# Kernel tuning notes

Measured on AMD Instinct MI355X. Metric: run time of the kernel, lower is better.

Reference implementation:

```python
import jax, jax.numpy as jnp
import numpy as np


def setup_inputs() -> dict:
    key = jax.random.key(0)
    k1, k2, k3, k4 = jax.random.split(key, 4)
    B, N_LEAVES, D_IN, L, C = 64, 512, 512, 5, 4
    n_nodes = 2 * N_LEAVES - 1  # heap layout: node i has children 2i+1, 2i+2
    h = jax.random.normal(k1, (B, n_nodes, D_IN), dtype=jnp.float32)
    W = jax.random.normal(k2, (D_IN, L * C), dtype=jnp.float32) * (1.0 / np.sqrt(D_IN))
    b = jax.random.normal(k3, (L * C,), dtype=jnp.float32) * 0.02
    trans = jax.random.normal(k4, (L, L, L, C, C, C), dtype=jnp.float32) * 0.1
    return {"h": h, "W": W, "b": b, "trans": trans}


def reference(h, W, b, trans):
    """Batched inside algorithm of BinaryTreeLatentVariable.forward.

    h: [B, n_nodes, D] node hidden states (complete binary tree, heap order).
    Returns root inside score [B, L, C].
    """
    B, n_nodes, _ = h.shape
    L = trans.shape[0]
    C = trans.shape[3]
    n_leaves = (n_nodes + 1) // 2
    depth = int(np.log2(n_leaves))

    # Emission: state_weight_layer applied to every node at once.
    sw = (h @ W + b).reshape(B, n_nodes, L, C)  # [B, N, L, C]

    # Leaves: in_weight = state_weight. Internal slots overwritten bottom-up.
    in_w = sw
    for d in range(depth - 1, -1, -1):  # level-synchronous, bottom-up
        start, end = 2 ** d - 1, 2 ** (d + 1) - 1  # internal nodes of this level
        l = in_w[:, 2 * start + 1:2 * end:2]        # [B, m, L, C] left children
        r = in_w[:, 2 * start + 2:2 * end + 1:2]    # [B, m, L, C] right children
        p = sw[:, start:end]                        # [B, m, L, C] parent emission
        # score[b,m, pL,lL,rL, pc,lc,rc]
        score = (p[:, :, :, None, None, :, None, None]
                 + l[:, :, None, :, None, None, :, None]
                 + r[:, :, None, None, :, None, None, :]
                 + trans)
        new = jax.nn.logsumexp(score, axis=(3, 4, 6, 7))  # marginalize children
        in_w = in_w.at[:, start:end].set(new)
    return in_w[:, 0]  # root inside score [B, L, C]
```

## Files before the change

kernel.cpp:

```cpp
#include <hip/hip_runtime.h>
#include <hip/hip_bf16.h>
#include <math.h>

#define NB      64
#define NNODES  1023
#define LC      20
#define DIN     512
#define NROWS   (NB * NNODES)
#define ET_PAD  404

#define BM      64
#define SCP     21

typedef unsigned short u16;
typedef short bf16x8 __attribute__((ext_vector_type(8)));
typedef float f32x4  __attribute__((ext_vector_type(4)));

__device__ __forceinline__ u16 f2bf(float f) {
    unsigned x = __float_as_uint(f);
    return (u16)((x + 0x7FFFu + ((x >> 16) & 1u)) >> 16);
}

__global__ __launch_bounds__(256) void prep_kernel(
    const float* __restrict__ trans, const float* __restrict__ W,
    float* __restrict__ ET, u16* __restrict__ Bfrag)
{
    int t = blockIdx.x * 256 + threadIdx.x;
    if (t < 8000) {
        int q   = t % 20;
        int rem = t / 20;
        int j   = rem % 20;
        int i   = rem / 20;
        int ll = i >> 2, cl = i & 3;
        int lr = j >> 2, cr = j & 3;
        int lp = q >> 2, cp = q & 3;
        int src = ((((lp * 5 + ll) * 5 + lr) * 4 + cp) * 4 + cl) * 4 + cr;
        ET[q * ET_PAD + i * 20 + j] = expf(trans[src]);
    }
    if (t < 1280) {
        int col, kb;
        if (t < 1024) {
            int lane = t & 63, cg = t >> 6;
            col = lane & 15;
            kb  = cg * 32 + ((lane >> 4) & 3) * 8;
        } else {
            int idx = t - 1024;
            int cg = idx >> 4, g = (idx >> 2) & 3, c = idx & 3;
            col = 16 + c;
            kb  = cg * 32 + g * 8;
        }
        unsigned e[8];
        #pragma unroll
        for (int j = 0; j < 8; ++j)
            e[j] = (unsigned)f2bf(W[(kb + j) * LC + col]);
        uint4 v;
        v.x = e[0] | (e[1] << 16); v.y = e[2] | (e[3] << 16);
        v.z = e[4] | (e[5] << 16); v.w = e[6] | (e[7] << 16);
        ((uint4*)Bfrag)[t] = v;
    }
}

__global__ __launch_bounds__(256, 5) void gemm_kernel(
    const float* __restrict__ h, const u16* __restrict__ Bfrag,
    const float* __restrict__ bias, float* __restrict__ buf)
{
    __shared__ uint4 Bs[1280];
    __shared__ float scT[BM * SCP];
    const int t    = threadIdx.x;
    const int lane = t & 63;
    const int wv   = t >> 6;
    const size_t row0 = (size_t)blockIdx.x * BM;

    Bs[t] = ((const uint4*)Bfrag)[t];
    Bs[t + 256] = ((const uint4*)Bfrag)[t + 256];
    Bs[t + 512] = ((const uint4*)Bfrag)[t + 512];
    Bs[t + 768] = ((const uint4*)Bfrag)[t + 768];
    Bs[t + 1024] = ((const uint4*)Bfrag)[t + 1024];

    const float4* ap4 = (const float4*)
        (h + (row0 + wv * 16 + (lane & 15)) * DIN + ((lane >> 4) << 3));

    f32x4 acc0 = {0.f,0.f,0.f,0.f}, acc1 = {0.f,0.f,0.f,0.f};
    const uint4 z4 = make_uint4(0u, 0u, 0u, 0u);

    float4 pa0 = ap4[0], pb0 = ap4[1];
    float4 pa1 = ap4[8], pb1 = ap4[9];

    asm volatile("s_waitcnt lgkmcnt(0)" ::: "memory");
    __builtin_amdgcn_s_barrier();

    #pragma unroll
    for (int c = 0; c < 16; ++c) {
        float4 x0, x1;
        if (c & 1) { x0 = pa1; x1 = pb1; }
        else       { x0 = pa0; x1 = pb0; }
        if (c + 2 < 16) {
            if (c & 1) { pa1 = ap4[(c + 2) * 8]; pb1 = ap4[(c + 2) * 8 + 1]; }
            else       { pa0 = ap4[(c + 2) * 8]; pb0 = ap4[(c + 2) * 8 + 1]; }
        }
        unsigned e0 = (unsigned)f2bf(x0.x) | ((unsigned)f2bf(x0.y) << 16);
        unsigned e1 = (unsigned)f2bf(x0.z) | ((unsigned)f2bf(x0.w) << 16);
        unsigned e2 = (unsigned)f2bf(x1.x) | ((unsigned)f2bf(x1.y) << 16);
        unsigned e3 = (unsigned)f2bf(x1.z) | ((unsigned)f2bf(x1.w) << 16);
        uint4 au = make_uint4(e0, e1, e2, e3);
        bf16x8 af = __builtin_bit_cast(bf16x8, au);

        uint4 b0 = Bs[c * 64 + lane];
        uint4 b1 = Bs[1024 + c * 16 + ((lane >> 4) << 2) + (lane & 3)];
        if ((lane & 15) >= 4) b1 = z4;

        acc0 = __builtin_amdgcn_mfma_f32_16x16x32_bf16(
            af, __builtin_bit_cast(bf16x8, b0), acc0, 0, 0, 0);
        acc1 = __builtin_amdgcn_mfma_f32_16x16x32_bf16(
            af, __builtin_bit_cast(bf16x8, b1), acc1, 0, 0, 0);
    }

    {
        int col0 = lane & 15;
        int r0   = wv * 16 + ((lane >> 4) << 2);
        float bv0 = bias[col0];
        #pragma unroll
        for (int p = 0; p < 4; ++p)
            scT[(r0 + p) * SCP + col0] = acc0[p] + bv0;
        if (col0 < 4) {
            float bv1 = bias[16 + col0];
            #pragma unroll
            for (int p = 0; p < 4; ++p)
                scT[(r0 + p) * SCP + 16 + col0] = acc1[p] + bv1;
        }
    }
    asm volatile("s_waitcnt lgkmcnt(0)" ::: "memory");
    __builtin_amdgcn_s_barrier();
    {
        float4* dst = (float4*)(buf + row0 * LC);
        int f0 = t * 4;
        float4 o;
        o.x = scT[((f0 + 0) / 20) * SCP + (f0 + 0) % 20];
        o.y = scT[((f0 + 1) / 20) * SCP + (f0 + 1) % 20];
        o.z = scT[((f0 + 2) / 20) * SCP + (f0 + 2) % 20];
        o.w = scT[((f0 + 3) / 20) * SCP + (f0 + 3) % 20];
        dst[t] = o;
        if (t < 64) {
            int p = 256 + t, g0 = p * 4;
            float4 o2;
            o2.x = scT[((g0 + 0) / 20) * SCP + (g0 + 0) % 20];
            o2.y = scT[((g0 + 1) / 20) * SCP + (g0 + 1) % 20];
            o2.z = scT[((g0 + 2) / 20) * SCP + (g0 + 2) % 20];
            o2.w = scT[((g0 + 3) / 20) * SCP + (g0 + 3) % 20];
            dst[p] = o2;
        }
    }
}

__device__ __forceinline__ void level_body(
    float* __restrict__ buf, const float* __restrict__ et,
    float* __restrict__ out, int bi, int node, int q)
{
    size_t pbase = ((size_t)bi * NNODES + node) * LC;
    size_t lbase = ((size_t)bi * NNODES + 2 * node + 1) * LC;

    float l[LC], r[LC];
    const float4* l4 = (const float4*)(buf + lbase);
    const float4* r4 = (const float4*)(buf + lbase + LC);
    #pragma unroll
    for (int v = 0; v < 5; ++v) {
        float4 lv = l4[v], rv = r4[v];
        l[4*v+0] = lv.x; l[4*v+1] = lv.y; l[4*v+2] = lv.z; l[4*v+3] = lv.w;
        r[4*v+0] = rv.x; r[4*v+1] = rv.y; r[4*v+2] = rv.z; r[4*v+3] = rv.w;
    }
    float maxl = l[0], maxr = r[0];
    #pragma unroll
    for (int i = 1; i < LC; ++i) {
        maxl = fmaxf(maxl, l[i]);
        maxr = fmaxf(maxr, r[i]);
    }
    float el[LC], er[LC];
    #pragma unroll
    for (int i = 0; i < LC; ++i) {
        el[i] = __expf(l[i] - maxl);
        er[i] = __expf(r[i] - maxr);
    }

    const float4* etq = (const float4*)(et + q * ET_PAD);
    float s = 0.f;
    #pragma unroll
    for (int i = 0; i < LC; ++i) {
        float4 e0 = etq[i*5+0], e1 = etq[i*5+1], e2 = etq[i*5+2],
               e3 = etq[i*5+3], e4 = etq[i*5+4];
        float d0 = 0.f, d1 = 0.f;
        d0 = fmaf(e0.x, er[0],  d0); d1 = fmaf(e0.y, er[1],  d1);
        d0 = fmaf(e0.z, er[2],  d0); d1 = fmaf(e0.w, er[3],  d1);
        d0 = fmaf(e1.x, er[4],  d0); d1 = fmaf(e1.y, er[5],  d1);
        d0 = fmaf(e1.z, er[6],  d0); d1 = fmaf(e1.w, er[7],  d1);
        d0 = fmaf(e2.x, er[8],  d0); d1 = fmaf(e2.y, er[9],  d1);
        d0 = fmaf(e2.z, er[10], d0); d1 = fmaf(e2.w, er[11], d1);
        d0 = fmaf(e3.x, er[12], d0); d1 = fmaf(e3.y, er[13], d1);
        d0 = fmaf(e3.z, er[14], d0); d1 = fmaf(e3.w, er[15], d1);
        d0 = fmaf(e4.x, er[16], d0); d1 = fmaf(e4.y, er[17], d1);
        d0 = fmaf(e4.z, er[18], d0); d1 = fmaf(e4.w, er[19], d1);
        s = fmaf(el[i], d0 + d1, s);
    }

    float val = buf[pbase + q] + maxl + maxr + __logf(s);
    buf[pbase + q] = val;
    if (out) out[(size_t)bi * LC + q] = val;
}

__global__ __launch_bounds__(256) void level_kernel(
    float* __restrict__ buf, const float* __restrict__ ETg,
    int start, int count)
{
    __shared__ float et[LC * ET_PAD];
    for (int idx = threadIdx.x; idx < LC * ET_PAD / 4; idx += 256)
        ((float4*)et)[idx] = ((const float4*)ETg)[idx];
    __syncthreads();

    int t  = blockIdx.x * 256 + threadIdx.x;
    int pj = t / LC;
    int q  = t - pj * LC;
    if (pj >= NB * count) return;
    int bi   = pj / count;
    int node = start + (pj - bi * count);
    level_body(buf, et, nullptr, bi, node, q);
}

__global__ __launch_bounds__(640) void tail_kernel(
    float* __restrict__ buf, const float* __restrict__ ETg,
    float* __restrict__ out)
{
    __shared__ float et[LC * ET_PAD];
    for (int idx = threadIdx.x; idx < LC * ET_PAD / 4; idx += 640)
        ((float4*)et)[idx] = ((const float4*)ETg)[idx];
    __syncthreads();

    const int bi = blockIdx.x;
    for (int d = 6; d >= 0; --d) {
        int count = 1 << d;
        int start = count - 1;
        int total = count * LC;
        for (int base = 0; base < total; base += 640) {
            int idx = base + (int)threadIdx.x;
            if (idx < total) {
                int node = start + idx / LC;
                int q    = idx % LC;
                level_body(buf, et, (d == 0) ? out : nullptr, bi, node, q);
            }
        }
        __syncthreads();
    }
}

extern "C" void kernel_launch(void* const* d_in, const int* in_sizes, int n_in,
                              void* d_out, int out_size, void* d_ws, size_t ws_size,
                              hipStream_t stream)
{
    const float* h     = (const float*)d_in[0];
    const float* W     = (const float*)d_in[1];
    const float* bias  = (const float*)d_in[2];
    const float* trans = (const float*)d_in[3];

    char* ws = (char*)d_ws;
    float* ET    = (float*)(ws);
    u16*   Bfrag = (u16*)(ws + 32768);
    float* buf   = (float*)(ws + 32768 + 24576);

    prep_kernel<<<32, 256, 0, stream>>>(trans, W, ET, Bfrag);

    gemm_kernel<<<NROWS / BM, 256, 0, stream>>>(h, Bfrag, bias, buf);

    for (int d = 8; d >= 7; --d) {
        int count = 1 << d;
        int start = count - 1;
        int T = NB * count * LC;
        level_kernel<<<(T + 255) / 256, 256, 0, stream>>>(buf, ET, start, count);
    }
    tail_kernel<<<NB, 640, 0, stream>>>(buf, ET, (float*)d_out);
}
```

Measured before the change: 74.11 us.

## Stage GEMM A tiles through LDS with async global_load_lds triple buffering

The GEMM kernel now loads the fp32 h tiles directly into a triple-buffered, XOR-swizzled LDS ring using global_load_lds, two chunks ahead, instead of prefetching into registers. The B fragments are also copied to LDS with direct global-to-LDS loads. The aim is to overlap HBM streaming of h with compute and free registers. The cost is a barrier every chunk, extra LDS traffic and a lower occupancy hint in the launch bounds.

After: 73.70 us. About the same (-0.6%).

```diff
diff --git a/kernel.cpp b/kernel.cpp
--- a/kernel.cpp
+++ b/kernel.cpp
@@ -19,6 +19,12 @@
 __device__ __forceinline__ u16 f2bf(float f) {
     unsigned x = __float_as_uint(f);
     return (u16)((x + 0x7FFFu + ((x >> 16) & 1u)) >> 16);
+}
+
+__device__ __forceinline__ void gload_lds16(const void* g, void* l) {
+    __builtin_amdgcn_global_load_lds(
+        (const __attribute__((address_space(1))) unsigned*)g,
+        (__attribute__((address_space(3))) unsigned*)l, 16, 0, 0);
 }
 
 __global__ __launch_bounds__(256) void prep_kernel(
@@ -60,10 +66,11 @@
     }
 }
 
-__global__ __launch_bounds__(256, 5) void gemm_kernel(
+__global__ __launch_bounds__(256, 3) void gemm_kernel(
     const float* __restrict__ h, const u16* __restrict__ Bfrag,
     const float* __restrict__ bias, float* __restrict__ buf)
 {
+    __shared__ float As[3][BM][32];
     __shared__ uint4 Bs[1280];
     __shared__ float scT[BM * SCP];
     const int t    = threadIdx.x;
@@ -71,33 +78,53 @@
     const int wv   = t >> 6;
     const size_t row0 = (size_t)blockIdx.x * BM;
 
-    Bs[t] = ((const uint4*)Bfrag)[t];
-    Bs[t + 256] = ((const uint4*)Bfrag)[t + 256];
-    Bs[t + 512] = ((const uint4*)Bfrag)[t + 512];
-    Bs[t + 768] = ((const uint4*)Bfrag)[t + 768];
-    Bs[t + 1024] = ((const uint4*)Bfrag)[t + 1024];
-
-    const float4* ap4 = (const float4*)
-        (h + (row0 + wv * 16 + (lane & 15)) * DIN + ((lane >> 4) << 3));
+    {
+        const char* bsrc = (const char*)Bfrag;
+        char* bdst = (char*)Bs;
+        #pragma unroll
+        for (int k = 0; k < 5; ++k) {
+            int slice = wv * 5 + k;
+            gload_lds16(bsrc + slice * 1024 + lane * 16, bdst + slice * 1024);
+        }
+    }
+
+    const int s0 = t, s1 = t + 256;
+    const int r0s = s0 >> 3, j0s = s0 & 7;
+    const int r1s = s1 >> 3, j1s = s1 & 7;
+    const float* g0 = h + (row0 + r0s) * DIN + ((j0s ^ (r0s & 7)) << 2);
+    const float* g1 = h + (row0 + r1s) * DIN + ((j1s ^ (r1s & 7)) << 2);
+    char* const asB = (char*)As;
+    const int d0 = (0 * 256 + wv * 64) * 16;
+    const int d1 = (1 * 256 + wv * 64) * 16;
+
+#define STAGE(B, C) {                                                         \
+    char* _lb = asB + (B) * 8192;                                             \
+    gload_lds16(g0 + (C) * 32, _lb + d0);                                     \
+    gload_lds16(g1 + (C) * 32, _lb + d1); }
+
+    STAGE(0, 0)
+    STAGE(1, 1)
+    asm volatile("s_waitcnt vmcnt(2) lgkmcnt(0)" ::: "memory");
+    __builtin_amdgcn_s_barrier();
 
     f32x4 acc0 = {0.f,0.f,0.f,0.f}, acc1 = {0.f,0.f,0.f,0.f};
     const uint4 z4 = make_uint4(0u, 0u, 0u, 0u);
-
-    float4 pa0 = ap4[0], pb0 = ap4[1];
-    float4 pa1 = ap4[8], pb1 = ap4[9];
-
-    asm volatile("s_waitcnt lgkmcnt(0)" ::: "memory");
-    __builtin_amdgcn_s_barrier();
+    const int R  = wv * 16 + (lane & 15);
+    const int xr = R & 7;
+    const int jb = (lane >> 4) << 1;
+    const int aoff0 = R * 128 + ((jb ^ xr) << 4);
+    const int aoff1 = R * 128 + (((jb | 1) ^ xr) << 4);
 
     #pragma unroll
     for (int c = 0; c < 16; ++c) {
-        float4 x0, x1;
-        if (c & 1) { x0 = pa1; x1 = pb1; }
-        else       { x0 = pa0; x1 = pb0; }
+        const int cur = c % 3;
         if (c + 2 < 16) {
-            if (c & 1) { pa1 = ap4[(c + 2) * 8]; pb1 = ap4[(c + 2) * 8 + 1]; }
-            else       { pa0 = ap4[(c + 2) * 8]; pb0 = ap4[(c + 2) * 8 + 1]; }
-        }
+            const int nxt = (c + 2) % 3;
+            STAGE(nxt, c + 2)
+        }
+        const char* ab = asB + cur * 8192;
+        float4 x0 = *(const float4*)(ab + aoff0);
+        float4 x1 = *(const float4*)(ab + aoff1);
         unsigned e0 = (unsigned)f2bf(x0.x) | ((unsigned)f2bf(x0.y) << 16);
         unsigned e1 = (unsigned)f2bf(x0.z) | ((unsigned)f2bf(x0.w) << 16);
         unsigned e2 = (unsigned)f2bf(x1.x) | ((unsigned)f2bf(x1.y) << 16);
@@ -113,7 +140,17 @@
             af, __builtin_bit_cast(bf16x8, b0), acc0, 0, 0, 0);
         acc1 = __builtin_amdgcn_mfma_f32_16x16x32_bf16(
             af, __builtin_bit_cast(bf16x8, b1), acc1, 0, 0, 0);
-    }
+
+        if (c < 15) {
+            if (c + 2 < 16) {
+                asm volatile("s_waitcnt vmcnt(2) lgkmcnt(0)" ::: "memory");
+            } else {
+                asm volatile("s_waitcnt vmcnt(0) lgkmcnt(0)" ::: "memory");
+            }
+            __builtin_amdgcn_s_barrier();
+        }
+    }
+#undef STAGE
 
     {
         int col0 = lane & 15;
@@ -129,8 +166,7 @@
                 scT[(r0 + p) * SCP + 16 + col0] = acc1[p] + bv1;
         }
     }
-    asm volatile("s_waitcnt lgkmcnt(0)" ::: "memory");
-    __builtin_amdgcn_s_barrier();
+    __syncthreads();
     {
         float4* dst = (float4*)(buf + row0 * LC);
         int f0 = t * 4;
@@ -141,12 +177,12 @@
         o.w = scT[((f0 + 3) / 20) * SCP + (f0 + 3) % 20];
         dst[t] = o;
         if (t < 64) {
-            int p = 256 + t, g0 = p * 4;
+            int p = 256 + t, g4 = p * 4;
             float4 o2;
-            o2.x = scT[((g0 + 0) / 20) * SCP + (g0 + 0) % 20];
-            o2.y = scT[((g0 + 1) / 20) * SCP + (g0 + 1) % 20];
-            o2.z = scT[((g0 + 2) / 20) * SCP + (g0 + 2) % 20];
-            o2.w = scT[((g0 + 3) / 20) * SCP + (g0 + 3) % 20];
+            o2.x = scT[((g4 + 0) / 20) * SCP + (g4 + 0) % 20];
+            o2.y = scT[((g4 + 1) / 20) * SCP + (g4 + 1) % 20];
+            o2.z = scT[((g4 + 2) / 20) * SCP + (g4 + 2) % 20];
+            o2.w = scT[((g4 + 3) / 20) * SCP + (g4 + 3) % 20];
             dst[p] = o2;
         }
     }
```
